# Optimization experiments

Measured on AMD Instinct MI355X. Metric: run time of the kernel, lower is better.

## Reference

```python
import jax, jax.numpy as jnp
import numpy as np
import math

B, S, D, H = 2, 2048, 768, 12
HD = D // H


def setup_inputs() -> dict:
    key = jax.random.key(0)
    ks = jax.random.split(key, 9)
    scale = 1.0 / math.sqrt(D)
    x = jax.random.normal(ks[0], (B, S, D), dtype=jnp.float32)
    # causal mask: True where attention is allowed (query i attends to key j<=i)
    mask = jnp.tril(jnp.ones((S, S), dtype=bool))[None, None]  # [1,1,S,S]
    wq = jax.random.normal(ks[1], (D, D), dtype=jnp.float32) * scale
    bq = jnp.zeros((D,), dtype=jnp.float32)
    wk = jax.random.normal(ks[2], (D, D), dtype=jnp.float32) * scale
    bk = jnp.zeros((D,), dtype=jnp.float32)
    wv = jax.random.normal(ks[3], (D, D), dtype=jnp.float32) * scale
    bv = jnp.zeros((D,), dtype=jnp.float32)
    wo = jax.random.normal(ks[4], (D, D), dtype=jnp.float32) * scale
    bo = jnp.zeros((D,), dtype=jnp.float32)
    return {"x": x, "mask": mask, "wq": wq, "bq": bq, "wk": wk, "bk": bk,
            "wv": wv, "bv": bv, "wo": wo, "bo": bo}


def reference(x, mask, wq, bq, wk, bk, wv, bv, wo, bo):
    b, s, d = x.shape
    # projections (flax Linear: y = x @ kernel + bias)
    q = (x @ wq + bq).reshape(b, s, H, HD).transpose(0, 2, 1, 3)  # [b,h,s,hd]
    k = (x @ wk + bk).reshape(b, s, H, HD).transpose(0, 2, 1, 3)
    v = (x @ wv + bv).reshape(b, s, H, HD).transpose(0, 2, 1, 3)
    scores = jnp.einsum('bhqd,bhkd->bhqk', q, k) / math.sqrt(HD)  # [b,h,s,s]
    scores = jnp.where(mask, scores, -jnp.inf)
    attn = jax.nn.softmax(scores, axis=-1)
    out = jnp.einsum('bhqk,bhkd->bhqd', attn, v)  # [b,h,s,hd]
    out = out.transpose(0, 2, 1, 3).reshape(b, s, d)
    return out @ wo + bo
```

## Files before the change

### kernel.cpp

```cpp
#include <hip/hip_runtime.h>
#include <math.h>

#define BATCH 2
#define SEQ   2048
#define DMODEL 768
#define NHEAD 12
#define HDIM  64

typedef unsigned short u16;
typedef __attribute__((ext_vector_type(8))) short bf16x8;
typedef __attribute__((ext_vector_type(4))) float f32x4;
typedef __attribute__((ext_vector_type(16))) float f32x16;
typedef __attribute__((ext_vector_type(8))) unsigned short us8;
typedef __attribute__((ext_vector_type(4))) unsigned short us4;

__device__ __forceinline__ u16 f2bf(float f) {
    union { float f; unsigned u; } v; v.f = f;
    unsigned u = v.u;
    u += 0x7fff + ((u >> 16) & 1);
    return (u16)(u >> 16);
}

__device__ __forceinline__ float fexp2(float x) {
#if __has_builtin(__builtin_amdgcn_exp2f)
    return __builtin_amdgcn_exp2f(x);
#else
    return exp2f(x);
#endif
}

__device__ __forceinline__ void g2l16(const void* g, void* l) {
    __builtin_amdgcn_global_load_lds(
        (const __attribute__((address_space(1))) unsigned int*)g,
        (__attribute__((address_space(3))) unsigned int*)(unsigned int)(unsigned long long)(uintptr_t)l,
        16, 0, 0);
}

__global__ __launch_bounds__(256) void prep(const float* __restrict__ x,
                                            const float* __restrict__ w0,
                                            const float* __restrict__ w1,
                                            const float* __restrict__ w2,
                                            const float* __restrict__ w3,
                                            u16* __restrict__ xb,
                                            u16* __restrict__ Wt_all) {
    __shared__ float t[32][33];
    const int bid = blockIdx.x;
    if (bid < 3072) {
        int i = bid * 256 + threadIdx.x;
        float4 v = ((const float4*)x)[i];
        us4 o;
        o.x = f2bf(v.x); o.y = f2bf(v.y); o.z = f2bf(v.z); o.w = f2bf(v.w);
        *(us4*)&xb[(size_t)i * 4] = o;
    } else {
        const int wid = bid - 3072;
        const int z  = wid / 576;
        const int rr = wid % 576;
        const int by = rr / 24, bx = rr % 24;
        const float* W = z == 0 ? w0 : z == 1 ? w1 : z == 2 ? w2 : w3;
        u16* Wt = Wt_all + (size_t)z * DMODEL * DMODEL;

        int tx = threadIdx.x & 31, ty = threadIdx.x >> 5;
        int xg = bx * 32 + tx;
        #pragma unroll
        for (int j = 0; j < 32; j += 8)
            t[ty + j][tx] = W[(size_t)(by * 32 + ty + j) * DMODEL + xg];
        __syncthreads();
        int x2 = by * 32 + tx;
        #pragma unroll
        for (int j = 0; j < 32; j += 8)
            Wt[(size_t)(bx * 32 + ty + j) * DMODEL + x2] = f2bf(t[tx][ty + j]);
    }
}

__global__ __launch_bounds__(256) void gemm_qkv(
    const u16* __restrict__ xb, const u16* __restrict__ WtQK,
    const u16* __restrict__ WtV,
    const float* __restrict__ bq, const float* __restrict__ bk,
    const float* __restrict__ bv,
    u16* __restrict__ QK, u16* __restrict__ Vt) {

    __shared__ __align__(16) u16 Sb[3][224 * 32];

    const int tid  = threadIdx.x;
    const int lane = tid & 63;
    const int w    = tid >> 6;
    const int quad = lane >> 4, l16 = lane & 15;
    const int wm   = w >> 1, wn = w & 1;
    const int braw = (int)blockIdx.x;
    const int b    = (braw & 7) * 96 + (braw >> 3);
    const bool qk  = b < 512;

    const int m0 = qk ? (b >> 4) * 128 : (((b - 512) & 7) * 96);
    const int n0 = qk ? (b & 15) * 96  : (((b - 512) >> 3) * 128);

    auto rowbase = [&](int row) -> const u16* {
        if (qk) return row < 128 ? xb   + (size_t)(m0 + row) * DMODEL
                                 : WtQK + (size_t)(n0 + row - 128) * DMODEL;
        return row < 96 ? WtV + (size_t)(m0 + row) * DMODEL
                        : xb  + (size_t)(n0 + row - 96) * DMODEL;
    };
    const int c0 = tid, c1 = tid + 256, c2 = tid + 512, c3 = (tid & 127) + 768;
    const u16* gp0 = rowbase(c0 >> 2) + (c0 & 3) * 8;
    const u16* gp1 = rowbase(c1 >> 2) + (c1 & 3) * 8;
    const u16* gp2 = rowbase(c2 >> 2) + (c2 & 3) * 8;
    const u16* gp3 = rowbase(c3 >> 2) + (c3 & 3) * 8;
    const bool four = tid < 128;

    auto STAGE = [&](int buf) {
        u16* L = Sb[buf];
        g2l16(gp0, L + c0 * 8);
        g2l16(gp1, L + c1 * 8);
        g2l16(gp2, L + c2 * 8);
        if (four) g2l16(gp3, L + c3 * 8);
        gp0 += 32; gp1 += 32; gp2 += 32; gp3 += 32;
    };

    STAGE(0); STAGE(1);
    int cur = 0, nb = 2;

    if (qk) {
        f32x4 acc[4][3] = {};
        for (int it = 0; it < 24; ++it) {
            if (it < 23) {
                if (w < 2) asm volatile("s_waitcnt vmcnt(4)" ::: "memory");
                else       asm volatile("s_waitcnt vmcnt(3)" ::: "memory");
            } else         asm volatile("s_waitcnt vmcnt(0)" ::: "memory");
            __builtin_amdgcn_s_barrier();
            if (it < 22) { STAGE(nb); nb = nb == 2 ? 0 : nb + 1; }

            const u16* As = Sb[cur];
            const u16* Bs = Sb[cur] + 128 * 32;
            bf16x8 af[4], bfr[3];
            #pragma unroll
            for (int i = 0; i < 4; ++i)
                af[i] = *(const bf16x8*)&As[(wm * 64 + i * 16 + l16) * 32 + quad * 8];
            #pragma unroll
            for (int j = 0; j < 3; ++j)
                bfr[j] = *(const bf16x8*)&Bs[(wn * 48 + j * 16 + l16) * 32 + quad * 8];
            #pragma unroll
            for (int i = 0; i < 4; ++i)
                #pragma unroll
                for (int j = 0; j < 3; ++j)
                    acc[i][j] = __builtin_amdgcn_mfma_f32_16x16x32_bf16(af[i], bfr[j], acc[i][j], 0, 0, 0);
            cur = cur == 2 ? 0 : cur + 1;
        }
        const size_t n_elem = (size_t)BATCH * SEQ * DMODEL;
        #pragma unroll
        for (int j = 0; j < 3; ++j) {
            const int n     = n0 + wn * 48 + j * 16 + l16;
            const int which = n / 768;
            const int nn    = n - which * 768;
            const float bias  = (which == 0 ? bq : bk)[nn];
            const float scale = (which == 0) ? 0.18033688011112043f : 1.0f;
            const int h = nn >> 6, hd = nn & 63;
            u16* outw = QK + (size_t)which * n_elem;
            #pragma unroll
            for (int i = 0; i < 4; ++i) {
                const int mbase = m0 + wm * 64 + i * 16 + quad * 4;
                #pragma unroll
                for (int r = 0; r < 4; ++r) {
                    const int m  = mbase + r;
                    const int b_ = m >> 11, s_ = m & 2047;
                    outw[(size_t)((b_ * NHEAD + h) * SEQ + s_) * HDIM + hd] =
                        f2bf((acc[i][j][r] + bias) * scale);
                }
            }
        }
    } else {
        f32x4 acc[3][4] = {};
        for (int it = 0; it < 24; ++it) {
            if (it < 23) {
                if (w < 2) asm volatile("s_waitcnt vmcnt(4)" ::: "memory");
                else       asm volatile("s_waitcnt vmcnt(3)" ::: "memory");
            } else         asm volatile("s_waitcnt vmcnt(0)" ::: "memory");
            __builtin_amdgcn_s_barrier();
            if (it < 22) { STAGE(nb); nb = nb == 2 ? 0 : nb + 1; }

            const u16* As = Sb[cur];
            const u16* Bs = Sb[cur] + 96 * 32;
            bf16x8 af[3], bfr[4];
            #pragma unroll
            for (int i = 0; i < 3; ++i)
                af[i] = *(const bf16x8*)&As[(wm * 48 + i * 16 + l16) * 32 + quad * 8];
            #pragma unroll
            for (int j = 0; j < 4; ++j)
                bfr[j] = *(const bf16x8*)&Bs[(wn * 64 + j * 16 + l16) * 32 + quad * 8];
            #pragma unroll
            for (int i = 0; i < 3; ++i)
                #pragma unroll
                for (int j = 0; j < 4; ++j)
                    acc[i][j] = __builtin_amdgcn_mfma_f32_16x16x32_bf16(af[i], bfr[j], acc[i][j], 0, 0, 0);
            cur = cur == 2 ? 0 : cur + 1;
        }
        #pragma unroll
        for (int i = 0; i < 3; ++i) {
            const int rbase = m0 + wm * 48 + i * 16 + quad * 4;
            #pragma unroll
            for (int r = 0; r < 4; ++r) {
                const int row_g = rbase + r;
                const float bias = bv[row_g];
                const int h = row_g >> 6, hd = row_g & 63;
                #pragma unroll
                for (int j = 0; j < 4; ++j) {
                    const int col_g = n0 + wn * 64 + j * 16 + l16;
                    const int b_ = col_g >> 11, s_ = col_g & 2047;
                    Vt[(size_t)((b_ * NHEAD + h) * HDIM + hd) * SEQ + s_] =
                        f2bf(acc[i][j][r] + bias);
                }
            }
        }
    }
}

__global__ __launch_bounds__(256) void gemm_out(
    const u16* __restrict__ Ag, const u16* __restrict__ Bt,
    const float* __restrict__ bo, float* __restrict__ out) {

    __shared__ __align__(16) u16 Sb[3][128 * 32];

    const int tid  = threadIdx.x;
    const int lane = tid & 63;
    const int w    = tid >> 6;
    const int quad = lane >> 4, l16 = lane & 15;
    const int wm   = w >> 1, wn = w & 1;

    const int braw = (int)blockIdx.x;
    const int sx   = (braw & 7) * 96 + (braw >> 3);
    const int m0 = (sx / 12) * 64, n0 = (sx % 12) * 64;

    const int c0 = tid, c1 = tid + 256;
    auto rowbase = [&](int row) -> const u16* {
        return row < 64 ? Ag + (size_t)(m0 + row) * DMODEL
                        : Bt + (size_t)(n0 + row - 64) * DMODEL;
    };
    const u16* gp0 = rowbase(c0 >> 2) + (c0 & 3) * 8;
    const u16* gp1 = rowbase(c1 >> 2) + (c1 & 3) * 8;

    auto STAGE = [&](int buf) {
        g2l16(gp0, Sb[buf] + c0 * 8);
        g2l16(gp1, Sb[buf] + c1 * 8);
        gp0 += 32; gp1 += 32;
    };

    STAGE(0); STAGE(1);
    int cur = 0, nb = 2;

    f32x4 acc[2][2] = {};
    for (int it = 0; it < 24; ++it) {
        if (it < 23) asm volatile("s_waitcnt vmcnt(2)" ::: "memory");
        else         asm volatile("s_waitcnt vmcnt(0)" ::: "memory");
        __builtin_amdgcn_s_barrier();
        if (it < 22) { STAGE(nb); nb = nb == 2 ? 0 : nb + 1; }

        const u16* As = Sb[cur];
        const u16* Bs = Sb[cur] + 64 * 32;
        bf16x8 af[2], bfr[2];
        #pragma unroll
        for (int i = 0; i < 2; ++i)
            af[i] = *(const bf16x8*)&As[(wm * 32 + i * 16 + l16) * 32 + quad * 8];
        #pragma unroll
        for (int j = 0; j < 2; ++j)
            bfr[j] = *(const bf16x8*)&Bs[(wn * 32 + j * 16 + l16) * 32 + quad * 8];
        #pragma unroll
        for (int i = 0; i < 2; ++i)
            #pragma unroll
            for (int j = 0; j < 2; ++j)
                acc[i][j] = __builtin_amdgcn_mfma_f32_16x16x32_bf16(af[i], bfr[j], acc[i][j], 0, 0, 0);
        cur = cur == 2 ? 0 : cur + 1;
    }

    #pragma unroll
    for (int i = 0; i < 2; ++i) {
        const int mbase = m0 + wm * 32 + i * 16 + quad * 4;
        #pragma unroll
        for (int r = 0; r < 4; ++r) {
            const int m = mbase + r;
            #pragma unroll
            for (int j = 0; j < 2; ++j) {
                const int n = n0 + wn * 32 + j * 16 + l16;
                out[(size_t)m * DMODEL + n] = acc[i][j][r] + bo[n];
            }
        }
    }
}

__global__ __launch_bounds__(256) void flash_attn_mfma(
    const u16* __restrict__ Q, const u16* __restrict__ K,
    const u16* __restrict__ Vt, u16* __restrict__ A) {

    __shared__ __align__(16) u16 Kl[3][64 * 64];
    __shared__ __align__(16) u16 Vl[3][64 * 64];

    const int tid  = threadIdx.x;
    const int lane = tid & 63;
    const int w    = tid >> 6;
    const int l32  = lane & 31;
    const int hi   = lane >> 5;
    const int qh   = w & 1;
    const int kh   = w >> 1;

    const int b0  = (int)blockIdx.x;
    const int xcd = b0 & 7, p = b0 >> 3;
    const int cs  = p & 31, rr = p >> 5;
    const int t   = (rr == 0) ? cs : (rr == 1) ? (63 - cs) : (64 + cs);
    const int j   = 31 - t / 3;
    const int bh  = 3 * xcd + (t % 3);
    const int tc  = j + 1;

    const size_t base = (size_t)bh * SEQ * HDIM;
    const u16* Qg = Q + base;
    const u16* Kg = K + base;
    const u16* Vg = Vt + base;

    const int wq0 = j * 64 + qh * 32;
    const int qg  = wq0 + l32;

    bf16x8 qf[4];
    #pragma unroll
    for (int c = 0; c < 4; ++c)
        qf[c] = *(const bf16x8*)&Qg[(size_t)qg * 64 + 16 * c + 8 * hi];

    f32x16 o0 = {}, o1 = {};
    float l_acc = 0.f;

    const int ch0 = tid, ch1 = tid + 256;
    const int r0 = ch0 >> 3, lc0 = (ch0 & 7) ^ (r0 & 7);
    const int r1 = ch1 >> 3, lc1 = (ch1 & 7) ^ (r1 & 7);
    const u16* kp0 = Kg + (size_t)r0 * 64 + lc0 * 8;
    const u16* kp1 = Kg + (size_t)r1 * 64 + lc1 * 8;
    const u16* vp0 = Vg + (size_t)r0 * SEQ + lc0 * 8;
    const u16* vp1 = Vg + (size_t)r1 * SEQ + lc1 * 8;

    auto STAGE = [&](int buf) {
        g2l16(kp0, &Kl[buf][ch0 * 8]);
        g2l16(kp1, &Kl[buf][ch1 * 8]);
        g2l16(vp0, &Vl[buf][ch0 * 8]);
        g2l16(vp1, &Vl[buf][ch1 * 8]);
        kp0 += 64 * 64; kp1 += 64 * 64;
        vp0 += 64;      vp1 += 64;
    };

    STAGE(0);
    if (tc > 1) STAGE(1);

    int cur = 0, nb = 2;
    const int cx = l32 & 7;
    for (int t2 = 0; t2 < tc; ++t2) {
        if (t2 + 1 < tc) asm volatile("s_waitcnt vmcnt(4)" ::: "memory");
        else             asm volatile("s_waitcnt vmcnt(0)" ::: "memory");
        __builtin_amdgcn_s_barrier();
        if (t2 + 2 < tc) { STAGE(nb); nb = (nb == 2) ? 0 : nb + 1; }

        const bool live = !(t2 == tc - 1 && qh == 0 && kh == 1);
        if (live) {
            const u16* Kc = Kl[cur];
            const u16* Vc = Vl[cur];
            const int j0 = t2 * 64;

            f32x16 s = {};
            __builtin_amdgcn_s_setprio(1);
            #pragma unroll
            for (int c = 0; c < 4; ++c) {
                bf16x8 kf = *(const bf16x8*)&Kc[(32 * kh + l32) * 64 + (((2 * c + hi) ^ cx) * 8)];
                s = __builtin_amdgcn_mfma_f32_32x32x16_bf16(kf, qf[c], s, 0, 0, 0);
            }
            __builtin_amdgcn_s_setprio(0);

            if (t2 == tc - 1) {
                #pragma unroll
                for (int r = 0; r < 16; ++r) {
                    const int key = j0 + 32 * kh + (r & 3) + 8 * (r >> 2) + 4 * hi;
                    if (key > qg) s[r] = -INFINITY;
                }
            }

            #pragma unroll
            for (int r = 0; r < 16; ++r) s[r] = fexp2(s[r]);
            float ps = 0.f;
            #pragma unroll
            for (int r = 0; r < 16; ++r) ps += s[r];
            l_acc += ps;

            bf16x8 pa[2];
            #pragma unroll
            for (int kw = 0; kw < 2; ++kw) {
                const int m0i = 2 * kw;
                unsigned a0l, a0h, a1l, a1h;
                asm("v_cvt_pk_bf16_f32 %0, %1, %2" : "=v"(a0l) : "v"(s[4 * m0i + 0]), "v"(s[4 * m0i + 1]));
                asm("v_cvt_pk_bf16_f32 %0, %1, %2" : "=v"(a0h) : "v"(s[4 * m0i + 2]), "v"(s[4 * m0i + 3]));
                asm("v_cvt_pk_bf16_f32 %0, %1, %2" : "=v"(a1l) : "v"(s[4 * (m0i + 1) + 0]), "v"(s[4 * (m0i + 1) + 1]));
                asm("v_cvt_pk_bf16_f32 %0, %1, %2" : "=v"(a1h) : "v"(s[4 * (m0i + 1) + 2]), "v"(s[4 * (m0i + 1) + 3]));
                asm("v_permlane32_swap_b32 %0, %1" : "+v"(a0l), "+v"(a1l));
                asm("v_permlane32_swap_b32 %0, %1" : "+v"(a0h), "+v"(a1h));
                union { unsigned u[4]; bf16x8 v; } pu;
                pu.u[0] = a0l; pu.u[1] = a0h; pu.u[2] = a1l; pu.u[3] = a1h;
                pa[kw] = pu.v;
            }

            __builtin_amdgcn_s_setprio(1);
            #pragma unroll
            for (int kw = 0; kw < 2; ++kw) {
                const int lc = ((4 * kh + 2 * kw + hi) ^ cx) * 8;
                bf16x8 vf0 = *(const bf16x8*)&Vc[l32 * 64 + lc];
                bf16x8 vf1 = *(const bf16x8*)&Vc[(32 + l32) * 64 + lc];
                o0 = __builtin_amdgcn_mfma_f32_32x32x16_bf16(vf0, pa[kw], o0, 0, 0, 0);
                o1 = __builtin_amdgcn_mfma_f32_32x32x16_bf16(vf1, pa[kw], o1, 0, 0, 0);
            }
            __builtin_amdgcn_s_setprio(0);
        }

        cur = (cur == 2) ? 0 : cur + 1;
    }

    l_acc += __shfl_xor(l_acc, 32);

    __syncthreads();

    float* ob = (float*)Kl;
    float* lb = (float*)Vl;
    if (kh == 1) {
        #pragma unroll
        for (int r = 0; r < 16; ++r) {
            ob[qh * 2048 + r * 64 + lane]        = o0[r];
            ob[qh * 2048 + (16 + r) * 64 + lane] = o1[r];
        }
        lb[qh * 64 + lane] = l_acc;
    }
    __syncthreads();

    if (kh == 0) {
        #pragma unroll
        for (int r = 0; r < 16; ++r) {
            o0[r] += ob[qh * 2048 + r * 64 + lane];
            o1[r] += ob[qh * 2048 + (16 + r) * 64 + lane];
        }
        const float inv = 1.0f / (l_acc + lb[qh * 64 + lane]);

        u16* Ot = ((u16*)Vl) + 256 + qh * 2304;
        #pragma unroll
        for (int r = 0; r < 16; ++r) {
            const int d = (r & 3) + 8 * (r >> 2) + 4 * hi;
            Ot[l32 * 72 + d]      = f2bf(o0[r] * inv);
            Ot[l32 * 72 + 32 + d] = f2bf(o1[r] * inv);
        }
        const int row = lane >> 1, d0 = (lane & 1) * 32;
        const int b_ = bh / NHEAD, h_ = bh % NHEAD;
        u16* dst = A + ((size_t)(b_ * SEQ + wq0 + row)) * DMODEL + h_ * HDIM + d0;
        #pragma unroll
        for (int k2 = 0; k2 < 4; ++k2)
            *(us8*)&dst[k2 * 8] = *(const us8*)&Ot[row * 72 + d0 + k2 * 8];
    }
}

extern "C" void kernel_launch(void* const* d_in, const int* in_sizes, int n_in,
                              void* d_out, int out_size, void* d_ws, size_t ws_size,
                              hipStream_t stream) {
    const float* x  = (const float*)d_in[0];
    const float* wq = (const float*)d_in[2];
    const float* bq = (const float*)d_in[3];
    const float* wk = (const float*)d_in[4];
    const float* bk = (const float*)d_in[5];
    const float* wv = (const float*)d_in[6];
    const float* bv = (const float*)d_in[7];
    const float* wo = (const float*)d_in[8];
    const float* bo = (const float*)d_in[9];
    float* out = (float*)d_out;

    const size_t n_elem = (size_t)BATCH * SEQ * DMODEL;
    const size_t w_elem = (size_t)DMODEL * DMODEL;

    u16* xb     = (u16*)d_ws;
    u16* Wt_all = xb + n_elem;
    u16* Qw     = Wt_all + 4 * w_elem;
    u16* Vtw    = Qw + 2 * n_elem;
    u16* Aw     = Vtw + n_elem;

    dim3 blk(256);

    prep<<<dim3(3072 + 2304), blk, 0, stream>>>(x, wq, wk, wv, wo, xb, Wt_all);

    gemm_qkv<<<dim3(768), blk, 0, stream>>>(xb, Wt_all, Wt_all + 2 * w_elem,
                                            bq, bk, bv, Qw, Vtw);

    flash_attn_mfma<<<dim3(768), blk, 0, stream>>>(Qw, Qw + n_elem, Vtw, Aw);

    gemm_out<<<dim3(768), blk, 0, stream>>>(Aw, Wt_all + 3 * w_elem, bo, out);
}
```

Measured before the change: 155.4 us.

## Enlarge flash attention blocks to 128 queries with 512 threads; raise MFMA priority in GEMMs

The attention kernel now runs 512-thread blocks that each cover 128 query rows (four query waves times two key halves), so every staged K/V tile is shared by twice as many queries and the grid shrinks to 384 blocks. Causal masking and liveness are now decided per wave from the key-tile offset, and the block-to-work mapping and LDS reduction layout are reworked to fit. The GEMM kernels also wrap their MFMA loops in s_setprio to favour the math waves. In exchange, fewer and larger blocks may cost occupancy and balance across the triangular causal workload, and more waves sit idle on diagonal tiles.

```diff
diff --git a/kernel.cpp b/kernel.cpp
--- a/kernel.cpp
+++ b/kernel.cpp
@@ -137,11 +137,13 @@
             #pragma unroll
             for (int j = 0; j < 3; ++j)
                 bfr[j] = *(const bf16x8*)&Bs[(wn * 48 + j * 16 + l16) * 32 + quad * 8];
+            __builtin_amdgcn_s_setprio(1);
             #pragma unroll
             for (int i = 0; i < 4; ++i)
                 #pragma unroll
                 for (int j = 0; j < 3; ++j)
                     acc[i][j] = __builtin_amdgcn_mfma_f32_16x16x32_bf16(af[i], bfr[j], acc[i][j], 0, 0, 0);
+            __builtin_amdgcn_s_setprio(0);
             cur = cur == 2 ? 0 : cur + 1;
         }
         const size_t n_elem = (size_t)BATCH * SEQ * DMODEL;
@@ -185,11 +187,13 @@
             #pragma unroll
             for (int j = 0; j < 4; ++j)
                 bfr[j] = *(const bf16x8*)&Bs[(wn * 64 + j * 16 + l16) * 32 + quad * 8];
+            __builtin_amdgcn_s_setprio(1);
             #pragma unroll
             for (int i = 0; i < 3; ++i)
                 #pragma unroll
                 for (int j = 0; j < 4; ++j)
                     acc[i][j] = __builtin_amdgcn_mfma_f32_16x16x32_bf16(af[i], bfr[j], acc[i][j], 0, 0, 0);
+            __builtin_amdgcn_s_setprio(0);
             cur = cur == 2 ? 0 : cur + 1;
         }
         #pragma unroll
@@ -261,11 +265,13 @@
         #pragma unroll
         for (int j = 0; j < 2; ++j)
             bfr[j] = *(const bf16x8*)&Bs[(wn * 32 + j * 16 + l16) * 32 + quad * 8];
+        __builtin_amdgcn_s_setprio(1);
         #pragma unroll
         for (int i = 0; i < 2; ++i)
             #pragma unroll
             for (int j = 0; j < 2; ++j)
                 acc[i][j] = __builtin_amdgcn_mfma_f32_16x16x32_bf16(af[i], bfr[j], acc[i][j], 0, 0, 0);
+        __builtin_amdgcn_s_setprio(0);
         cur = cur == 2 ? 0 : cur + 1;
     }
 
@@ -284,7 +290,7 @@
     }
 }
 
-__global__ __launch_bounds__(256) void flash_attn_mfma(
+__global__ __launch_bounds__(512) void flash_attn_mfma(
     const u16* __restrict__ Q, const u16* __restrict__ K,
     const u16* __restrict__ Vt, u16* __restrict__ A) {
 
@@ -296,23 +302,25 @@
     const int w    = tid >> 6;
     const int l32  = lane & 31;
     const int hi   = lane >> 5;
-    const int qh   = w & 1;
-    const int kh   = w >> 1;
+    const int qh   = w & 3;
+    const int kh   = w >> 2;
 
     const int b0  = (int)blockIdx.x;
     const int xcd = b0 & 7, p = b0 >> 3;
-    const int cs  = p & 31, rr = p >> 5;
-    const int t   = (rr == 0) ? cs : (rr == 1) ? (63 - cs) : (64 + cs);
-    const int j   = 31 - t / 3;
-    const int bh  = 3 * xcd + (t % 3);
-    const int tc  = j + 1;
+    int rank;
+    if (p >= 16 && p < 32) rank = p - 16;
+    else if (p < 16)       rank = 16 + p;
+    else                   rank = 79 - p;
+    const int J   = 15 - rank / 3;
+    const int bh  = 3 * xcd + rank % 3;
+    const int tc  = 2 * J + 2;
 
     const size_t base = (size_t)bh * SEQ * HDIM;
     const u16* Qg = Q + base;
     const u16* Kg = K + base;
     const u16* Vg = Vt + base;
 
-    const int wq0 = j * 64 + qh * 32;
+    const int wq0 = J * 128 + qh * 32;
     const int qg  = wq0 + l32;
 
     bf16x8 qf[4];
@@ -323,39 +331,34 @@
     f32x16 o0 = {}, o1 = {};
     float l_acc = 0.f;
 
-    const int ch0 = tid, ch1 = tid + 256;
-    const int r0 = ch0 >> 3, lc0 = (ch0 & 7) ^ (r0 & 7);
-    const int r1 = ch1 >> 3, lc1 = (ch1 & 7) ^ (r1 & 7);
-    const u16* kp0 = Kg + (size_t)r0 * 64 + lc0 * 8;
-    const u16* kp1 = Kg + (size_t)r1 * 64 + lc1 * 8;
-    const u16* vp0 = Vg + (size_t)r0 * SEQ + lc0 * 8;
-    const u16* vp1 = Vg + (size_t)r1 * SEQ + lc1 * 8;
+    const int ch = tid;
+    const int r_ = ch >> 3, lc_ = (ch & 7) ^ (r_ & 7);
+    const u16* kp = Kg + (size_t)r_ * 64 + lc_ * 8;
+    const u16* vp = Vg + (size_t)r_ * SEQ + lc_ * 8;
 
     auto STAGE = [&](int buf) {
-        g2l16(kp0, &Kl[buf][ch0 * 8]);
-        g2l16(kp1, &Kl[buf][ch1 * 8]);
-        g2l16(vp0, &Vl[buf][ch0 * 8]);
-        g2l16(vp1, &Vl[buf][ch1 * 8]);
-        kp0 += 64 * 64; kp1 += 64 * 64;
-        vp0 += 64;      vp1 += 64;
+        g2l16(kp, &Kl[buf][ch * 8]);
+        g2l16(vp, &Vl[buf][ch * 8]);
+        kp += 64 * 64;
+        vp += 64;
     };
 
     STAGE(0);
-    if (tc > 1) STAGE(1);
+    STAGE(1);
 
     int cur = 0, nb = 2;
     const int cx = l32 & 7;
     for (int t2 = 0; t2 < tc; ++t2) {
-        if (t2 + 1 < tc) asm volatile("s_waitcnt vmcnt(4)" ::: "memory");
+        if (t2 + 1 < tc) asm volatile("s_waitcnt vmcnt(2)" ::: "memory");
         else             asm volatile("s_waitcnt vmcnt(0)" ::: "memory");
         __builtin_amdgcn_s_barrier();
         if (t2 + 2 < tc) { STAGE(nb); nb = (nb == 2) ? 0 : nb + 1; }
 
-        const bool live = !(t2 == tc - 1 && qh == 0 && kh == 1);
+        const int kbase = t2 * 64 + 32 * kh;
+        const bool live = (kbase <= wq0 + 31);
         if (live) {
             const u16* Kc = Kl[cur];
             const u16* Vc = Vl[cur];
-            const int j0 = t2 * 64;
 
             f32x16 s = {};
             __builtin_amdgcn_s_setprio(1);
@@ -366,10 +369,10 @@
             }
             __builtin_amdgcn_s_setprio(0);
 
-            if (t2 == tc - 1) {
+            if (kbase + 31 > wq0) {
                 #pragma unroll
                 for (int r = 0; r < 16; ++r) {
-                    const int key = j0 + 32 * kh + (r & 3) + 8 * (r >> 2) + 4 * hi;
+                    const int key = kbase + (r & 3) + 8 * (r >> 2) + 4 * hi;
                     if (key > qg) s[r] = -INFINITY;
                 }
             }
@@ -416,27 +419,32 @@
 
     __syncthreads();
 
-    float* ob = (float*)Kl;
-    float* lb = (float*)Vl;
+    float* obA = (float*)Kl;
+    float* obB = (float*)Vl;
+    float* lb  = ((float*)Vl) + 4096;
     if (kh == 1) {
         #pragma unroll
         for (int r = 0; r < 16; ++r) {
-            ob[qh * 2048 + r * 64 + lane]        = o0[r];
-            ob[qh * 2048 + (16 + r) * 64 + lane] = o1[r];
+            obA[qh * 1024 + r * 64 + lane] = o0[r];
+            obB[qh * 1024 + r * 64 + lane] = o1[r];
         }
         lb[qh * 64 + lane] = l_acc;
     }
     __syncthreads();
 
+    float inv = 0.f;
     if (kh == 0) {
         #pragma unroll
         for (int r = 0; r < 16; ++r) {
-            o0[r] += ob[qh * 2048 + r * 64 + lane];
-            o1[r] += ob[qh * 2048 + (16 + r) * 64 + lane];
-        }
-        const float inv = 1.0f / (l_acc + lb[qh * 64 + lane]);
-
-        u16* Ot = ((u16*)Vl) + 256 + qh * 2304;
+            o0[r] += obA[qh * 1024 + r * 64 + lane];
+            o1[r] += obB[qh * 1024 + r * 64 + lane];
+        }
+        inv = 1.0f / (l_acc + lb[qh * 64 + lane]);
+    }
+    __syncthreads();
+
+    if (kh == 0) {
+        u16* Ot = ((u16*)Kl) + qh * 2304;
         #pragma unroll
         for (int r = 0; r < 16; ++r) {
             const int d = (r & 3) + 8 * (r >> 2) + 4 * hi;
@@ -482,7 +490,7 @@
     gemm_qkv<<<dim3(768), blk, 0, stream>>>(xb, Wt_all, Wt_all + 2 * w_elem,
                                             bq, bk, bv, Qw, Vtw);
 
-    flash_attn_mfma<<<dim3(768), blk, 0, stream>>>(Qw, Qw + n_elem, Vtw, Aw);
+    flash_attn_mfma<<<dim3(384), dim3(512), 0, stream>>>(Qw, Qw + n_elem, Vtw, Aw);
 
     gemm_out<<<dim3(768), blk, 0, stream>>>(Aw, Wt_all + 3 * w_elem, bo, out);
 }
```

Measured after the change: 164.6 us. 5.9% more time.
